# Kernel optimization log

Measured on AMD Instinct MI355X. Metric: run time of the kernel, lower is better.

The kernel has to match this reference:

```python
import jax, jax.numpy as jnp
import numpy as np

B, N, FN, FE, OUT = 64, 128, 64, 16, 128
S, VOCAB, EMB, LH = 1033, 1033, 50, 8
MOMO, SIDE, T = 200, 963, 3
LN_EPS, BN_EPS = 1e-12, 1e-5


def setup_inputs():
    key = jax.random.key(0)
    ks = iter(jax.random.split(key, 64))
    def nrm(shape, scale=0.05):
        return jax.random.normal(next(ks), shape, dtype=jnp.float32) * scale
    inp = {}
    inp['adjacency_1'] = (jax.random.uniform(next(ks), (B, N, N)) < 0.1).astype(jnp.float32)
    inp['nodes_1'] = nrm((B, N, FN), 1.0)
    inp['edges_1'] = nrm((B, N, N, FE), 1.0)
    inp['adjacency_2'] = (jax.random.uniform(next(ks), (B, N, N)) < 0.1).astype(jnp.float32)
    inp['nodes_2'] = nrm((B, N, FN), 1.0)
    inp['edges_2'] = nrm((B, N, N, FE), 1.0)
    inp['d1_momo_fts'] = nrm((B, MOMO), 1.0)
    inp['d2_momo_fts'] = nrm((B, MOMO), 1.0)
    inp['d1_protein_fts'] = jax.random.randint(next(ks), (B, S), 0, VOCAB)
    inp['d2_protein_fts'] = jax.random.randint(next(ks), (B, S), 0, VOCAB)
    inp['side_effect'] = nrm((B, SIDE), 1.0)
    inp['word_emb'] = nrm((VOCAB, EMB))
    inp['pos_emb'] = nrm((VOCAB, EMB))
    inp['ln_gamma'] = jnp.ones((EMB,), jnp.float32)
    inp['ln_beta'] = jnp.zeros((EMB,), jnp.float32)
    inp['W_ih'] = nrm((4 * LH, EMB))
    inp['W_hh'] = nrm((4 * LH, LH))
    inp['b_ih'] = jnp.zeros((4 * LH,), jnp.float32)
    inp['b_hh'] = jnp.zeros((4 * LH,), jnp.float32)
    inp['dec_W1'] = nrm((LH * S, 256))
    inp['dec_b1'] = jnp.zeros((256,), jnp.float32)
    inp['bn_gamma'] = jnp.ones((256,), jnp.float32)
    inp['bn_beta'] = jnp.zeros((256,), jnp.float32)
    inp['dec_W2'] = nrm((256, 45))
    inp['dec_b2'] = jnp.zeros((45,), jnp.float32)
    for g in ('1', '2'):
        inp['W_msg' + g] = nrm((FN, FN))
        inp['W_edge' + g] = nrm((FE, FN))
        inp['W_up' + g] = nrm((2 * FN, FN))
        inp['b_up' + g] = jnp.zeros((FN,), jnp.float32)
        inp['W_read' + g] = nrm((2 * FN, OUT))
        inp['b_read' + g] = jnp.zeros((OUT,), jnp.float32)
    inp['W_momo'] = nrm((MOMO, 45))
    inp['b_momo'] = jnp.zeros((45,), jnp.float32)
    inp['W_side'] = nrm((SIDE, 32))
    inp['b_side'] = jnp.zeros((32,), jnp.float32)
    inp['W_final'] = nrm((2 * (OUT + 45 + 45) + 32, 1))
    inp['b_final'] = jnp.zeros((1,), jnp.float32)
    return inp


def _mpnn(adj, nodes, edges, W_msg, W_edge, W_up, b_up, W_read, b_read):
    # Dense-masked equivalent of the padded neighbor/edge gather construction:
    # message[b,n] = sum_m adj[b,n,m] * (h[b,m] @ W_msg + e[b,n,m] @ W_edge)
    node_mask = adj.sum(-1) > 0  # [B,N] -- only connected nodes are updated
    edge_msg = jnp.einsum('bnm,bnmf,fk->bnk', adj, edges, W_edge)  # static over passes
    h = nodes
    for _ in range(T):
        msg = jnp.einsum('bnm,bmf,fk->bnk', adj, h, W_msg) + edge_msg
        upd = jax.nn.relu(jnp.concatenate([h, msg], -1) @ W_up + b_up)
        h = jnp.where(node_mask[..., None], upd, h)
    r = jax.nn.relu(jnp.concatenate([h, nodes], -1) @ W_read + b_read)  # [B,N,OUT]
    return jnp.einsum('bn,bnk->bk', node_mask.astype(h.dtype), r)


def _protein(ids, word_emb, pos_emb, ln_gamma, ln_beta, W_ih, W_hh, b_ih, b_hh,
             dec_W1, dec_b1, bn_gamma, bn_beta, dec_W2, dec_b2):
    x = word_emb[ids] + pos_emb[jnp.arange(S)][None]  # [B,S,EMB]
    u = x.mean(-1, keepdims=True)
    s = ((x - u) ** 2).mean(-1, keepdims=True)
    x = ln_gamma * (x - u) / jnp.sqrt(s + LN_EPS) + ln_beta
    def step(carry, xt):  # torch LSTM gate order: i, f, g, o
        h, c = carry
        gates = xt @ W_ih.T + b_ih + h @ W_hh.T + b_hh
        i, f, g, o = jnp.split(gates, 4, axis=-1)
        c = jax.nn.sigmoid(f) * c + jax.nn.sigmoid(i) * jnp.tanh(g)
        h = jax.nn.sigmoid(o) * jnp.tanh(c)
        return (h, c), h
    h0 = jnp.zeros((ids.shape[0], LH), jnp.float32)
    _, hs = jax.lax.scan(step, (h0, h0), jnp.swapaxes(x, 0, 1))  # [S,B,LH]
    p = jnp.swapaxes(hs, 0, 1).reshape(ids.shape[0], -1)  # [B, S*LH]
    p = jax.nn.relu(p @ dec_W1 + dec_b1)
    m, v = p.mean(0), p.var(0)  # BatchNorm1d in training mode (batch stats)
    p = bn_gamma * (p - m) / jnp.sqrt(v + BN_EPS) + bn_beta
    return p @ dec_W2 + dec_b2  # [B,45]


def reference(adjacency_1, nodes_1, edges_1, adjacency_2, nodes_2, edges_2,
              d1_momo_fts, d1_protein_fts, d2_momo_fts, d2_protein_fts, side_effect,
              word_emb, pos_emb, ln_gamma, ln_beta, W_ih, W_hh, b_ih, b_hh,
              dec_W1, dec_b1, bn_gamma, bn_beta, dec_W2, dec_b2,
              W_msg1, W_edge1, W_up1, b_up1, W_read1, b_read1,
              W_msg2, W_edge2, W_up2, b_up2, W_read2, b_read2,
              W_momo, b_momo, W_side, b_side, W_final, b_final):
    out1 = _mpnn(adjacency_1, nodes_1, edges_1, W_msg1, W_edge1, W_up1, b_up1, W_read1, b_read1)
    out2 = _mpnn(adjacency_2, nodes_2, edges_2, W_msg2, W_edge2, W_up2, b_up2, W_read2, b_read2)
    p1 = _protein(d1_protein_fts, word_emb, pos_emb, ln_gamma, ln_beta, W_ih, W_hh, b_ih, b_hh,
                  dec_W1, dec_b1, bn_gamma, bn_beta, dec_W2, dec_b2)
    p2 = _protein(d2_protein_fts, word_emb, pos_emb, ln_gamma, ln_beta, W_ih, W_hh, b_ih, b_hh,
                  dec_W1, dec_b1, bn_gamma, bn_beta, dec_W2, dec_b2)
    momo1 = d1_momo_fts @ W_momo + b_momo
    momo2 = d2_momo_fts @ W_momo + b_momo
    drug1 = jnp.concatenate([out1, p1, momo1], axis=1)
    drug2 = jnp.concatenate([out2, p2, momo2], axis=1)
    side = side_effect @ W_side + b_side
    feats = jnp.concatenate([drug1, drug2, side], axis=1)
    return feats @ W_final + b_final  # [B,1]
```

## Files before the change

kernel.cpp:

```cpp
#include <hip/hip_runtime.h>
#include <hip/hip_bf16.h>
#include <math.h>

#define Bb 64
#define Nn 128
#define FNf 64
#define Ss 1033
#define EMBe 50

typedef float f4 __attribute__((ext_vector_type(4)));
typedef float f2 __attribute__((ext_vector_type(2)));
typedef int   i4 __attribute__((ext_vector_type(4)));

#define HS_KSTRIDE 1036
#define HS_BSTRIDE 8288
#define HS_PSIZE   530432

constexpr size_t OFF_EMSG  = 2*524288 + 2*524288;
constexpr size_t OFF_MASK  = OFF_EMSG  + 2*524288;
constexpr size_t OFF_OUT12 = OFF_MASK  + 2*8192;
constexpr size_t OFF_PPRE  = OFF_OUT12 + 2*8192;
constexpr size_t OFF_PBN   = OFF_PPRE  + 2*16384;
constexpr size_t OFF_XW    = OFF_PBN   + 2*16384;
constexpr size_t OFF_HS    = OFF_XW    + 2*2115584;
constexpr size_t OFF_W2F   = OFF_HS    + 2*HS_PSIZE;
constexpr size_t OFF_WMF   = OFF_W2F   + 2*256;
constexpr size_t OFF_WSF   = OFF_WMF   + 2*200;
constexpr size_t OFF_CONST = OFF_WSF   + 964;
constexpr size_t OFF_COUNT = OFF_CONST + 4;
constexpr size_t OFF_NZ    = OFF_COUNT + 2*8192;
constexpr size_t OFF_AVAL  = OFF_NZ    + 2*524288;

__device__ inline f4 relu4(f4 v) {
  v[0] = fmaxf(v[0], 0.f); v[1] = fmaxf(v[1], 0.f);
  v[2] = fmaxf(v[2], 0.f); v[3] = fmaxf(v[3], 0.f);
  return v;
}

#define ROR16(x, n) __int_as_float(__builtin_amdgcn_update_dpp(0, __float_as_int(x), 0x120 + (n), 0xF, 0xF, true))

__global__ __launch_bounds__(256) void kA(
    const float* __restrict__ adj1, const float* __restrict__ adj2,
    const float* __restrict__ edges1, const float* __restrict__ edges2,
    const float* __restrict__ We1, const float* __restrict__ We2,
    const int* __restrict__ ids1, const int* __restrict__ ids2,
    const float* __restrict__ we, const float* __restrict__ pe,
    const float* __restrict__ lng, const float* __restrict__ lnb,
    const float* __restrict__ Wih, const float* __restrict__ bih,
    const float* __restrict__ bhh, float* __restrict__ ws) {
  int bid = blockIdx.x;
  int t = threadIdx.x;
  if (bid < 4096) {
    int g = bid >> 11;
    int w = t >> 6, lane = t & 63;
    int row = (bid & 2047) * 4 + w;
    const float* adj   = g ? adj2 : adj1;
    const float* edges = g ? edges2 : edges1;
    const float* We    = g ? We2 : We1;
    float* emsg  = ws + OFF_EMSG + (size_t)g * 524288;
    int*   cntg  = (int*)(ws + OFF_COUNT) + (size_t)g * 8192;
    int*   nz    = (int*)(ws + OFF_NZ)    + (size_t)g * 524288;
    float* aval  = ws + OFF_AVAL + (size_t)g * 524288;

    __shared__ int   lidx[4][64];
    __shared__ float lav[4][64];
    __shared__ float les[4][16];

    const float* arow = adj + (size_t)row * 128;
    float a0 = arow[lane], a1 = arow[64 + lane];
    unsigned long long m0 = __ballot(a0 != 0.f);
    unsigned long long m1 = __ballot(a1 != 0.f);
    int c0 = __popcll(m0);
    int cnt = c0 + __popcll(m1);
    unsigned long long below = ((unsigned long long)1 << lane) - 1ull;
    if (a0 != 0.f) { int pos = __popcll(m0 & below); if (pos < 64) { lidx[w][pos] = lane; lav[w][pos] = a0; } }
    if (a1 != 0.f) { int pos = c0 + __popcll(m1 & below); if (pos < 64) { lidx[w][pos] = lane + 64; lav[w][pos] = a1; } }
    int cc = cnt > 64 ? 64 : cnt;
    __syncthreads();

    nz[(size_t)row * 64 + lane]   = (lane < cc) ? lidx[w][lane] : 0;
    aval[(size_t)row * 64 + lane] = (lane < cc) ? lav[w][lane] : 0.f;

    int f = lane & 15, js = lane >> 4;
    float es = 0.f;
    const float* erow = edges + (size_t)row * 128 * 16;
    for (int j = js; j < cc; j += 4) es += lav[w][j] * erow[lidx[w][j] * 16 + f];
    es += __shfl_xor(es, 16);
    es += __shfl_xor(es, 32);
    if (lane < 16) les[w][lane] = es;
    __syncthreads();

    float acc = 0.f;
    #pragma unroll
    for (int ff = 0; ff < 16; ++ff) acc += les[w][ff] * We[ff * 64 + lane];
    emsg[(size_t)row * 64 + lane] = acc;
    if (lane == 0) cntg[row] = cc;
    return;
  }
  int bid6 = bid - 4096;
  int p = bid6 / 2066;
  int xb = bid6 % 2066;
  const int* ids = p ? ids2 : ids1;
  float* xw = ws + OFF_XW + (size_t)p * 2115584;
  __shared__ float wlds[1600];
  __shared__ float glds[50], blds[50], bs[32];
  __shared__ float xl6[8][52];
  for (int i = t; i < 1600; i += 256) wlds[i] = Wih[i];
  if (t < 50) { glds[t] = lng[t]; blds[t] = lnb[t]; }
  if (t < 32) bs[t] = bih[t] + bhh[t];
  __syncthreads();
  int grp = t >> 5, tl = t & 31;
  int newpos = (tl < 16) ? 2 * tl : 2 * tl - 31;
  const float L = 1.44269504088896f;
  float scale = (tl >= 16 && tl < 24) ? -2.f * L : -L;
  int q0 = xb * 32 + grp * 4;
  for (int qq = 0; qq < 4; ++qq) {
    int q = q0 + qq;
    int s = q % Ss;
    int id = ids[q];
    const float* wr = we + (size_t)id * 50;
    const float* pr = pe + (size_t)s * 50;
    float x1 = wr[tl] + pr[tl];
    bool has2 = (tl + 32) < 50;
    float x2 = has2 ? (wr[tl + 32] + pr[tl + 32]) : 0.f;
    float sm = x1 + x2, sq = x1 * x1 + x2 * x2;
    #pragma unroll
    for (int off = 16; off; off >>= 1) {
      sm += __shfl_xor(sm, off, 32);
      sq += __shfl_xor(sq, off, 32);
    }
    float u = sm * (1.f / 50.f);
    float var = fmaxf(sq * (1.f / 50.f) - u * u, 0.f);
    float rstd = rsqrtf(var + 1e-12f);
    xl6[grp][tl] = glds[tl] * (x1 - u) * rstd + blds[tl];
    if (has2) xl6[grp][tl + 32] = glds[tl + 32] * (x2 - u) * rstd + blds[tl + 32];
    __builtin_amdgcn_wave_barrier();
    float acc = bs[tl];
    #pragma unroll 10
    for (int k = 0; k < 50; ++k) acc += xl6[grp][k] * wlds[tl * 50 + k];
    xw[(size_t)q * 32 + newpos] = acc * scale;
    __builtin_amdgcn_wave_barrier();
  }
}

__global__ __launch_bounds__(256) void kB(
    const float* __restrict__ nodes1, const float* __restrict__ nodes2,
    const float* __restrict__ Wm1, const float* __restrict__ Wm2,
    const float* __restrict__ Wup1, const float* __restrict__ Wup2,
    const float* __restrict__ bup1, const float* __restrict__ bup2,
    const float* __restrict__ Wr1, const float* __restrict__ Wr2,
    const float* __restrict__ br1, const float* __restrict__ br2,
    const float* __restrict__ Whh, float* __restrict__ ws) {
  __shared__ __attribute__((aligned(16))) float hl[8192];
  __shared__ __attribute__((aligned(16))) float xl[8192];
  __shared__ __attribute__((aligned(16))) float wml[4096];
  __shared__ __attribute__((aligned(16))) float wbl[8192];
  int bid = blockIdx.x;
  int t = threadIdx.x;
  if (bid >= 128) {
    if (t >= 64) return;
    int idx = bid - 128;
    int p = idx >> 4, xb = idx & 15;
    const float* xw = ws + OFF_XW + (size_t)p * 2115584;
    float* hs = ws + OFF_HS + (size_t)p * HS_PSIZE;
    int lane16 = t & 15;
    int k = lane16 & 7;
    int half = lane16 >> 3;
    int b = xb * 4 + (t >> 4);
    const float* xwp = xw + (size_t)b * (Ss * 32) + lane16 * 2;
    float* hq = hs + (size_t)b * HS_BSTRIDE + (size_t)k * HS_KSTRIDE;
    const float L = 1.44269504088896f;
    int ga = half ? 8 + k : k;
    int gb = half ? 24 + k : 16 + k;
    float sb_scale = half ? -L : -2.f * L;
    float wa[8], wb[8];
    #pragma unroll
    for (int r = 0; r < 8; ++r) {
      int j = (k - r) & 7;
      wa[r] = -L * Whh[ga * 8 + j];
      wb[r] = sb_scale * Whh[gb * 8 + j];
    }
    float A = half ? 0.f : -4.f * L;
    float B = half ? 1.f : 2.f * L;
    float ho = 0.f, cs = 0.f;
    float q0v = 0.f, q1v = 0.f, q2v = 0.f, q3v = 0.f;

    f2 x[8];
    #pragma unroll
    for (int j = 0; j < 8; ++j) x[j] = *(const f2*)(xwp + (size_t)j * 32);
    const float* pf = xwp + 8 * 32;

    auto step = [&](f2 xc) {
      float h1 = ROR16(ho, 1);
      float h2 = ROR16(ho, 2);
      float h3 = ROR16(ho, 3);
      float h4 = ROR16(ho, 4);
      float h5 = ROR16(ho, 5);
      float h6 = ROR16(ho, 6);
      float h7 = ROR16(ho, 7);
      float a0 = fmaf(ho, wa[0], xc.x);
      float b0 = fmaf(ho, wb[0], xc.y);
      a0 = fmaf(h1, wa[1], a0);  b0 = fmaf(h1, wb[1], b0);
      a0 = fmaf(h2, wa[2], a0);  b0 = fmaf(h2, wb[2], b0);
      a0 = fmaf(h3, wa[3], a0);  b0 = fmaf(h3, wb[3], b0);
      float a1 = h4 * wa[4];     float b1 = h4 * wb[4];
      a1 = fmaf(h5, wa[5], a1);  b1 = fmaf(h5, wb[5], b1);
      a1 = fmaf(h6, wa[6], a1);  b1 = fmaf(h6, wb[6], b1);
      a1 = fmaf(h7, wa[7], a1);  b1 = fmaf(h7, wb[7], b1);
      float acc_a = a0 + a1;
      float acc_b = b0 + b1;
      float ea = __builtin_amdgcn_exp2f(acc_a);
      float sa = __builtin_amdgcn_rcpf(1.f + ea);
      float eb = __builtin_amdgcn_exp2f(acc_b);
      float tb = __builtin_amdgcn_rcpf(1.f + eb);
      float x_own = fmaf(sa * A, tb, sa * B);
      float x_oth = ROR16(x_own, 8);
      float t_oth = ROR16(tb, 8);
      float F  = half ? x_own : x_oth;
      float P2 = half ? x_oth : x_own;
      cs = fmaf(F, cs, P2);
      float e2 = __builtin_amdgcn_exp2f(cs);
      float tc = __builtin_amdgcn_rcpf(1.f + e2);
      float so = half ? tb : t_oth;
      ho = fmaf(so + so, tc, -so);
    };

    for (int g = 0; g < 129; ++g) {
      #pragma unroll
      for (int j = 0; j < 8; ++j) {
        f2 xc = x[j];
        x[j] = *(const f2*)(pf + j * 32);
        step(xc);
        if (j == 0 || j == 4) q0v = ho;
        else if (j == 1 || j == 5) q1v = ho;
        else if (j == 2 || j == 6) q2v = ho;
        else if (j == 3) { q3v = ho; if (!half) *(f4*)(hq + 0) = (f4){q0v, q1v, q2v, q3v}; }
        else { q3v = ho; if (!half) *(f4*)(hq + 4) = (f4){q0v, q1v, q2v, q3v}; }
      }
      pf += 256;
      hq += 8;
    }
    step(x[0]);
    if (!half) hq[0] = ho;
    return;
  }
  int g = bid >> 6, b = bid & 63;
  const float* nodes = g ? nodes2 : nodes1;
  const float* Wm  = g ? Wm2 : Wm1;
  const float* Wup = g ? Wup2 : Wup1;
  const float* bup = g ? bup2 : bup1;
  const float* Wr  = g ? Wr2 : Wr1;
  const float* br  = g ? br2 : br1;
  const float* emsg = ws + OFF_EMSG + (size_t)g * 524288;
  const int*   cntg = (const int*)(ws + OFF_COUNT) + (size_t)g * 8192;
  const int*   nz   = (const int*)(ws + OFF_NZ) + (size_t)g * 524288;
  const float* aval = ws + OFF_AVAL + (size_t)g * 524288;
  float* out12 = ws + OFF_OUT12 + (size_t)g * 8192;

  int col4 = (t & 15) * 4, rg = t >> 4;
  int r0 = rg * 8;
  for (int i = t; i < 4096; i += 256) wml[i] = Wm[i];
  for (int i = t; i < 8192; i += 256) wbl[i] = Wup[i];
  for (int i = t; i < 8192; i += 256) hl[i] = nodes[(size_t)b * 8192 + i];
  __syncthreads();

  for (int it = 0; it < 3; ++it) {
    {
      f4 acc[8];
      #pragma unroll
      for (int rr = 0; rr < 8; ++rr) acc[rr] = (f4){0.f, 0.f, 0.f, 0.f};
      for (int f0 = 0; f0 < 64; f0 += 4) {
        f4 h4[8];
        #pragma unroll
        for (int rr = 0; rr < 8; ++rr) h4[rr] = *(const f4*)&hl[(r0 + rr) * 64 + f0];
        #pragma unroll
        for (int ff = 0; ff < 4; ++ff) {
          f4 w4 = *(const f4*)&wml[(f0 + ff) * 64 + col4];
          #pragma unroll
          for (int rr = 0; rr < 8; ++rr) acc[rr] += h4[rr][ff] * w4;
        }
      }
      #pragma unroll
      for (int rr = 0; rr < 8; ++rr) *(f4*)&xl[(r0 + rr) * 64 + col4] = acc[rr];
    }
    __syncthreads();
    f4 msgv[8];
    #pragma unroll
    for (int rr = 0; rr < 8; ++rr) {
      int row = b * 128 + r0 + rr;
      f4 m = *(const f4*)&emsg[(size_t)row * 64 + col4];
      int cnt4 = (cntg[row] + 3) >> 2;
      const i4* nzr = (const i4*)(nz + (size_t)row * 64);
      const f4* avr = (const f4*)(aval + (size_t)row * 64);
      for (int j4 = 0; j4 < cnt4; ++j4) {
        i4 nq = nzr[j4];
        f4 aq = avr[j4];
        m += aq[0] * *(const f4*)&xl[nq[0] * 64 + col4];
        m += aq[1] * *(const f4*)&xl[nq[1] * 64 + col4];
        m += aq[2] * *(const f4*)&xl[nq[2] * 64 + col4];
        m += aq[3] * *(const f4*)&xl[nq[3] * 64 + col4];
      }
      msgv[rr] = m;
    }
    __syncthreads();
    #pragma unroll
    for (int rr = 0; rr < 8; ++rr) *(f4*)&xl[(r0 + rr) * 64 + col4] = msgv[rr];
    __syncthreads();
    {
      f4 u[8];
      #pragma unroll
      for (int rr = 0; rr < 8; ++rr) u[rr] = *(const f4*)&bup[col4];
      for (int f0 = 0; f0 < 64; f0 += 4) {
        f4 h4[8];
        #pragma unroll
        for (int rr = 0; rr < 8; ++rr) h4[rr] = *(const f4*)&hl[(r0 + rr) * 64 + f0];
        #pragma unroll
        for (int ff = 0; ff < 4; ++ff) {
          f4 w4 = *(const f4*)&wbl[(f0 + ff) * 64 + col4];
          #pragma unroll
          for (int rr = 0; rr < 8; ++rr) u[rr] += h4[rr][ff] * w4;
        }
      }
      for (int f0 = 0; f0 < 64; f0 += 4) {
        f4 m4[8];
        #pragma unroll
        for (int rr = 0; rr < 8; ++rr) m4[rr] = *(const f4*)&xl[(r0 + rr) * 64 + f0];
        #pragma unroll
        for (int ff = 0; ff < 4; ++ff) {
          f4 w4 = *(const f4*)&wbl[(64 + f0 + ff) * 64 + col4];
          #pragma unroll
          for (int rr = 0; rr < 8; ++rr) u[rr] += m4[rr][ff] * w4;
        }
      }
      __syncthreads();
      #pragma unroll
      for (int rr = 0; rr < 8; ++rr) {
        int row = b * 128 + r0 + rr;
        if (cntg[row] > 0) *(f4*)&hl[(r0 + rr) * 64 + col4] = relu4(u[rr]);
      }
    }
    __syncthreads();
  }

  for (int i = t; i < 8192; i += 256) xl[i] = nodes[(size_t)b * 8192 + i];
  __syncthreads();
  for (int kt = 0; kt < 2; ++kt) {
    for (int i = t; i < 8192; i += 256) {
      int f = i >> 6, c = i & 63;
      wbl[i] = Wr[f * 128 + kt * 64 + c];
    }
    __syncthreads();
    f4 part = {0.f, 0.f, 0.f, 0.f};
    {
      f4 u[8];
      #pragma unroll
      for (int rr = 0; rr < 8; ++rr) u[rr] = *(const f4*)&br[kt * 64 + col4];
      for (int f0 = 0; f0 < 64; f0 += 4) {
        f4 h4[8];
        #pragma unroll
        for (int rr = 0; rr < 8; ++rr) h4[rr] = *(const f4*)&hl[(r0 + rr) * 64 + f0];
        #pragma unroll
        for (int ff = 0; ff < 4; ++ff) {
          f4 w4 = *(const f4*)&wbl[(f0 + ff) * 64 + col4];
          #pragma unroll
          for (int rr = 0; rr < 8; ++rr) u[rr] += h4[rr][ff] * w4;
        }
      }
      for (int f0 = 0; f0 < 64; f0 += 4) {
        f4 n4[8];
        #pragma unroll
        for (int rr = 0; rr < 8; ++rr) n4[rr] = *(const f4*)&xl[(r0 + rr) * 64 + f0];
        #pragma unroll
        for (int ff = 0; ff < 4; ++ff) {
          f4 w4 = *(const f4*)&wbl[(64 + f0 + ff) * 64 + col4];
          #pragma unroll
          for (int rr = 0; rr < 8; ++rr) u[rr] += n4[rr][ff] * w4;
        }
      }
      #pragma unroll
      for (int rr = 0; rr < 8; ++rr) {
        int row = b * 128 + r0 + rr;
        if (cntg[row] > 0) part += relu4(u[rr]);
      }
    }
    *(f4*)&wml[rg * 64 + col4] = part;
    __syncthreads();
    for (int off = 8; off; off >>= 1) {
      if (rg < off) {
        f4 v = *(f4*)&wml[rg * 64 + col4] + *(f4*)&wml[(rg + off) * 64 + col4];
        *(f4*)&wml[rg * 64 + col4] = v;
      }
      __syncthreads();
    }
    if (rg == 0) *(f4*)&out12[(size_t)b * 128 + kt * 64 + col4] = *(f4*)&wml[col4];
    __syncthreads();
  }
}

__global__ __launch_bounds__(256) void kC(
    const float* __restrict__ W1,
    const float* __restrict__ W2, const float* __restrict__ b2,
    const float* __restrict__ Wm, const float* __restrict__ bm,
    const float* __restrict__ Wsd, const float* __restrict__ bsd,
    const float* __restrict__ Wf, const float* __restrict__ bf,
    float* __restrict__ ws) {
  int bid = blockIdx.x;
  int t = threadIdx.x;
  if (bid < 256) {
    int ks = bid & 31, jt = (bid >> 5) & 3, p = bid >> 7;
    const float* hs = ws + OFF_HS + (size_t)p * HS_PSIZE;
    float* pp = ws + OFF_PPRE + (size_t)p * 16384;
    int s0 = ks * 32;
    int s1 = (ks == 31) ? Ss : s0 + 32;
    int j0 = jt * 64;
    __shared__ __attribute__((aligned(16))) float hsl[4][768];
    __shared__ __attribute__((aligned(16))) float w1l[4][512];
    int jl = (t & 15) * 4, bb = t >> 4;
    f4 acc[4] = {};
    for (int sb = s0; sb < s1; sb += 4) {
      #pragma unroll
      for (int u = 0; u < 2; ++u) {
        int bk = t + 256 * u;
        int b = bk >> 3, k = bk & 7;
        f4 v = *(const f4*)&hs[(size_t)b * HS_BSTRIDE + (size_t)k * HS_KSTRIDE + sb];
        int c = b * 12 + k;
        hsl[0][c] = v[0]; hsl[1][c] = v[1]; hsl[2][c] = v[2]; hsl[3][c] = v[3];
      }
      #pragma unroll
      for (int u = 0; u < 2; ++u) {
        int idx = t + 256 * u;
        int ss = idx >> 7, l = (idx >> 4) & 7, jj = (idx & 15) * 4;
        int s = sb + ss;
        f4 wv = (s < Ss) ? *(const f4*)&W1[(size_t)(s * 8 + l) * 256 + j0 + jj]
                         : (f4){0.f, 0.f, 0.f, 0.f};
        *(f4*)&w1l[ss][l * 64 + jj] = wv;
      }
      __syncthreads();
      #pragma unroll
      for (int ss = 0; ss < 4; ++ss) {
        f4 r[4][2];
        #pragma unroll
        for (int i = 0; i < 4; ++i) {
          int b = bb + 16 * i;
          r[i][0] = *(const f4*)&hsl[ss][b * 12];
          r[i][1] = *(const f4*)&hsl[ss][b * 12 + 4];
        }
        #pragma unroll
        for (int l = 0; l < 8; ++l) {
          f4 wv = *(const f4*)&w1l[ss][l * 64 + jl];
          #pragma unroll
          for (int i = 0; i < 4; ++i) {
            float hv = (l < 4) ? r[i][0][l] : r[i][1][l - 4];
            acc[i] += hv * wv;
          }
        }
      }
      __syncthreads();
    }
    #pragma unroll
    for (int i = 0; i < 4; ++i) {
      int b = bb + 16 * i;
      float* dst = pp + (size_t)b * 256 + j0 + jl;
      atomicAdd(dst + 0, acc[i][0]); atomicAdd(dst + 1, acc[i][1]);
      atomicAdd(dst + 2, acc[i][2]); atomicAdd(dst + 3, acc[i][3]);
    }
    return;
  }
  __shared__ float wf[468];
  for (int i = t; i < 468; i += 256) wf[i] = Wf[i];
  __syncthreads();
  float* w2f = ws + OFF_W2F;
  float* wmf = ws + OFF_WMF;
  float* wsf = ws + OFF_WSF;
  float* cst = ws + OFF_CONST;
  {
    float a1 = 0.f, a2 = 0.f;
    for (int k = 0; k < 45; ++k) {
      float v = W2[t * 45 + k];
      a1 += v * wf[128 + k];
      a2 += v * wf[346 + k];
    }
    w2f[t] = a1; w2f[256 + t] = a2;
  }
  if (t < 200) {
    float a1 = 0.f, a2 = 0.f;
    for (int k = 0; k < 45; ++k) {
      float v = Wm[t * 45 + k];
      a1 += v * wf[173 + k];
      a2 += v * wf[391 + k];
    }
    wmf[t] = a1; wmf[200 + t] = a2;
  }
  for (int i = t; i < 963; i += 256) {
    float a = 0.f;
    for (int k = 0; k < 32; ++k) a += Wsd[i * 32 + k] * wf[436 + k];
    wsf[i] = a;
  }
  if (t == 0) {
    float cc = bf[0];
    for (int k = 0; k < 45; ++k)
      cc += b2[k] * (wf[128 + k] + wf[346 + k]) + bm[k] * (wf[173 + k] + wf[391 + k]);
    for (int k = 0; k < 32; ++k) cc += bsd[k] * wf[436 + k];
    cst[0] = cc;
  }
}

__global__ __launch_bounds__(256) void kD(
    const float* __restrict__ b1, const float* __restrict__ bng,
    const float* __restrict__ bnb,
    const float* __restrict__ d1m, const float* __restrict__ d2m,
    const float* __restrict__ se, const float* __restrict__ Wf,
    float* __restrict__ ws, float* __restrict__ out) {
  int b = blockIdx.x, t = threadIdx.x;
  const float* out12 = ws + OFF_OUT12;
  const float* pp0 = ws + OFF_PPRE;
  const float* pp1 = ws + OFF_PPRE + 16384;
  const float* w2f = ws + OFF_W2F;
  const float* wmf = ws + OFF_WMF;
  const float* wsf = ws + OFF_WSF;
  float bj = b1[t];
  float sm0 = 0.f, sq0 = 0.f, sm1 = 0.f, sq1 = 0.f;
  for (int bb = 0; bb < 64; ++bb) {
    float v0 = fmaxf(pp0[bb * 256 + t] + bj, 0.f);
    float v1 = fmaxf(pp1[bb * 256 + t] + bj, 0.f);
    sm0 += v0; sq0 += v0 * v0;
    sm1 += v1; sq1 += v1 * v1;
  }
  float m0 = sm0 * (1.f / 64.f);
  float var0 = fmaxf(sq0 * (1.f / 64.f) - m0 * m0, 0.f);
  float rstd0 = rsqrtf(var0 + 1e-5f);
  float sc0 = bng[t] * rstd0, sh0 = bnb[t] - m0 * sc0;
  float m1 = sm1 * (1.f / 64.f);
  float var1 = fmaxf(sq1 * (1.f / 64.f) - m1 * m1, 0.f);
  float rstd1 = rsqrtf(var1 + 1e-5f);
  float sc1 = bng[t] * rstd1, sh1 = bnb[t] - m1 * sc1;
  float val0 = sc0 * fmaxf(pp0[b * 256 + t] + bj, 0.f) + sh0;
  float val1 = sc1 * fmaxf(pp1[b * 256 + t] + bj, 0.f) + sh1;
  float acc = val0 * w2f[t] + val1 * w2f[256 + t];
  if (t < 128) {
    acc += out12[b * 128 + t] * Wf[t];
    acc += out12[8192 + b * 128 + t] * Wf[218 + t];
  }
  if (t < 200) {
    acc += d1m[b * 200 + t] * wmf[t];
    acc += d2m[b * 200 + t] * wmf[200 + t];
  }
  for (int i = t; i < 963; i += 256) acc += se[b * 963 + i] * wsf[i];
  __shared__ float red[256];
  red[t] = acc;
  __syncthreads();
  for (int off = 128; off; off >>= 1) {
    if (t < off) red[t] += red[t + off];
    __syncthreads();
  }
  if (t == 0) out[b] = red[0] + (ws + OFF_CONST)[0];
}

extern "C" void kernel_launch(void* const* d_in, const int* in_sizes, int n_in,
                              void* d_out, int out_size, void* d_ws, size_t ws_size,
                              hipStream_t stream) {
  const float* adj1  = (const float*)d_in[0];
  const float* nodes1= (const float*)d_in[1];
  const float* edges1= (const float*)d_in[2];
  const float* adj2  = (const float*)d_in[3];
  const float* nodes2= (const float*)d_in[4];
  const float* edges2= (const float*)d_in[5];
  const float* d1m   = (const float*)d_in[6];
  const float* d2m   = (const float*)d_in[7];
  const int*   ids1  = (const int*)d_in[8];
  const int*   ids2  = (const int*)d_in[9];
  const float* se    = (const float*)d_in[10];
  const float* we    = (const float*)d_in[11];
  const float* pe    = (const float*)d_in[12];
  const float* lng   = (const float*)d_in[13];
  const float* lnb   = (const float*)d_in[14];
  const float* Wih   = (const float*)d_in[15];
  const float* Whh   = (const float*)d_in[16];
  const float* bih   = (const float*)d_in[17];
  const float* bhh   = (const float*)d_in[18];
  const float* W1    = (const float*)d_in[19];
  const float* b1    = (const float*)d_in[20];
  const float* bng   = (const float*)d_in[21];
  const float* bnb   = (const float*)d_in[22];
  const float* W2    = (const float*)d_in[23];
  const float* b2    = (const float*)d_in[24];
  const float* Wm1   = (const float*)d_in[25];
  const float* We1   = (const float*)d_in[26];
  const float* Wup1  = (const float*)d_in[27];
  const float* bup1  = (const float*)d_in[28];
  const float* Wr1   = (const float*)d_in[29];
  const float* br1   = (const float*)d_in[30];
  const float* Wm2   = (const float*)d_in[31];
  const float* We2   = (const float*)d_in[32];
  const float* Wup2  = (const float*)d_in[33];
  const float* bup2  = (const float*)d_in[34];
  const float* Wr2   = (const float*)d_in[35];
  const float* br2   = (const float*)d_in[36];
  const float* Wmo   = (const float*)d_in[37];
  const float* bmo   = (const float*)d_in[38];
  const float* Wsd   = (const float*)d_in[39];
  const float* bsd   = (const float*)d_in[40];
  const float* Wf    = (const float*)d_in[41];
  const float* bf    = (const float*)d_in[42];
  float* ws = (float*)d_ws;
  float* out = (float*)d_out;

  hipMemsetAsync(ws + OFF_PPRE, 0, 2 * 16384 * sizeof(float), stream);

  kA<<<8228, 256, 0, stream>>>(adj1, adj2, edges1, edges2, We1, We2,
                               ids1, ids2, we, pe, lng, lnb, Wih, bih, bhh, ws);
  kB<<<160, 256, 0, stream>>>(nodes1, nodes2, Wm1, Wm2, Wup1, Wup2, bup1, bup2,
                              Wr1, Wr2, br1, br2, Whh, ws);
  kC<<<257, 256, 0, stream>>>(W1, W2, b2, Wmo, bmo, Wsd, bsd, Wf, bf, ws);
  kD<<<64, 256, 0, stream>>>(b1, bng, bnb, d1m, d2m, se, Wf, ws, out);
}
```

Before: 226.8 us.

## Overlap LSTM recurrence with decoder GEMM via progress flags; fold memset and fusion prep

The decoder W1 GEMM moves from a separate kernel into extra blocks of kB. These blocks spin on per-chunk progress counters that the LSTM recurrence blocks publish with release stores, so the GEMM can consume hidden states while the recurrence is still running. The small final-weight fusion precompute and the zeroing of the accumulation buffer move into extra kA blocks, which removes the memset and the kC launch. The price is spin-wait polling and a reliance on all 256 kB blocks being resident at once; without that the producer/consumer scheme could deadlock. The split-K tiling also goes from 32 to 12 chunks per slice, each covering more timesteps.

```diff
diff --git a/kernel.cpp b/kernel.cpp
--- a/kernel.cpp
+++ b/kernel.cpp
@@ -47,7 +47,12 @@
     const float* __restrict__ we, const float* __restrict__ pe,
     const float* __restrict__ lng, const float* __restrict__ lnb,
     const float* __restrict__ Wih, const float* __restrict__ bih,
-    const float* __restrict__ bhh, float* __restrict__ ws) {
+    const float* __restrict__ bhh,
+    const float* __restrict__ W2, const float* __restrict__ b2,
+    const float* __restrict__ Wm, const float* __restrict__ bm,
+    const float* __restrict__ Wsd, const float* __restrict__ bsd,
+    const float* __restrict__ Wf, const float* __restrict__ bf,
+    float* __restrict__ ws) {
   int bid = blockIdx.x;
   int t = threadIdx.x;
   if (bid < 4096) {
@@ -97,50 +102,100 @@
     if (lane == 0) cntg[row] = cc;
     return;
   }
-  int bid6 = bid - 4096;
-  int p = bid6 / 2066;
-  int xb = bid6 % 2066;
-  const int* ids = p ? ids2 : ids1;
-  float* xw = ws + OFF_XW + (size_t)p * 2115584;
-  __shared__ float wlds[1600];
-  __shared__ float glds[50], blds[50], bs[32];
-  __shared__ float xl6[8][52];
-  for (int i = t; i < 1600; i += 256) wlds[i] = Wih[i];
-  if (t < 50) { glds[t] = lng[t]; blds[t] = lnb[t]; }
-  if (t < 32) bs[t] = bih[t] + bhh[t];
-  __syncthreads();
-  int grp = t >> 5, tl = t & 31;
-  int newpos = (tl < 16) ? 2 * tl : 2 * tl - 31;
-  const float L = 1.44269504088896f;
-  float scale = (tl >= 16 && tl < 24) ? -2.f * L : -L;
-  int q0 = xb * 32 + grp * 4;
-  for (int qq = 0; qq < 4; ++qq) {
-    int q = q0 + qq;
-    int s = q % Ss;
-    int id = ids[q];
-    const float* wr = we + (size_t)id * 50;
-    const float* pr = pe + (size_t)s * 50;
-    float x1 = wr[tl] + pr[tl];
-    bool has2 = (tl + 32) < 50;
-    float x2 = has2 ? (wr[tl + 32] + pr[tl + 32]) : 0.f;
-    float sm = x1 + x2, sq = x1 * x1 + x2 * x2;
-    #pragma unroll
-    for (int off = 16; off; off >>= 1) {
-      sm += __shfl_xor(sm, off, 32);
-      sq += __shfl_xor(sq, off, 32);
-    }
-    float u = sm * (1.f / 50.f);
-    float var = fmaxf(sq * (1.f / 50.f) - u * u, 0.f);
-    float rstd = rsqrtf(var + 1e-12f);
-    xl6[grp][tl] = glds[tl] * (x1 - u) * rstd + blds[tl];
-    if (has2) xl6[grp][tl + 32] = glds[tl + 32] * (x2 - u) * rstd + blds[tl + 32];
-    __builtin_amdgcn_wave_barrier();
-    float acc = bs[tl];
-    #pragma unroll 10
-    for (int k = 0; k < 50; ++k) acc += xl6[grp][k] * wlds[tl * 50 + k];
-    xw[(size_t)q * 32 + newpos] = acc * scale;
-    __builtin_amdgcn_wave_barrier();
-  }
+  if (bid < 8228) {
+    int bid6 = bid - 4096;
+    int p = bid6 / 2066;
+    int xb = bid6 % 2066;
+    const int* ids = p ? ids2 : ids1;
+    float* xw = ws + OFF_XW + (size_t)p * 2115584;
+    __shared__ float wlds[1600];
+    __shared__ float glds[50], blds[50], bs[32];
+    __shared__ float xl6[8][52];
+    for (int i = t; i < 1600; i += 256) wlds[i] = Wih[i];
+    if (t < 50) { glds[t] = lng[t]; blds[t] = lnb[t]; }
+    if (t < 32) bs[t] = bih[t] + bhh[t];
+    __syncthreads();
+    int grp = t >> 5, tl = t & 31;
+    int newpos = (tl < 16) ? 2 * tl : 2 * tl - 31;
+    const float L = 1.44269504088896f;
+    float scale = (tl >= 16 && tl < 24) ? -2.f * L : -L;
+    int q0 = xb * 32 + grp * 4;
+    for (int qq = 0; qq < 4; ++qq) {
+      int q = q0 + qq;
+      int s = q % Ss;
+      int id = ids[q];
+      const float* wr = we + (size_t)id * 50;
+      const float* pr = pe + (size_t)s * 50;
+      float x1 = wr[tl] + pr[tl];
+      bool has2 = (tl + 32) < 50;
+      float x2 = has2 ? (wr[tl + 32] + pr[tl + 32]) : 0.f;
+      float sm = x1 + x2, sq = x1 * x1 + x2 * x2;
+      #pragma unroll
+      for (int off = 16; off; off >>= 1) {
+        sm += __shfl_xor(sm, off, 32);
+        sq += __shfl_xor(sq, off, 32);
+      }
+      float u = sm * (1.f / 50.f);
+      float var = fmaxf(sq * (1.f / 50.f) - u * u, 0.f);
+      float rstd = rsqrtf(var + 1e-12f);
+      xl6[grp][tl] = glds[tl] * (x1 - u) * rstd + blds[tl];
+      if (has2) xl6[grp][tl + 32] = glds[tl + 32] * (x2 - u) * rstd + blds[tl + 32];
+      __builtin_amdgcn_wave_barrier();
+      float acc = bs[tl];
+      #pragma unroll 10
+      for (int k = 0; k < 50; ++k) acc += xl6[grp][k] * wlds[tl * 50 + k];
+      xw[(size_t)q * 32 + newpos] = acc * scale;
+      __builtin_amdgcn_wave_barrier();
+    }
+    return;
+  }
+  if (bid == 8228) {
+    __shared__ float wf[468];
+    for (int i = t; i < 468; i += 256) wf[i] = Wf[i];
+    __syncthreads();
+    float* w2f = ws + OFF_W2F;
+    float* wmf = ws + OFF_WMF;
+    float* wsf = ws + OFF_WSF;
+    float* cst = ws + OFF_CONST;
+    {
+      float a1 = 0.f, a2 = 0.f;
+      for (int k = 0; k < 45; ++k) {
+        float v = W2[t * 45 + k];
+        a1 += v * wf[128 + k];
+        a2 += v * wf[346 + k];
+      }
+      w2f[t] = a1; w2f[256 + t] = a2;
+    }
+    if (t < 200) {
+      float a1 = 0.f, a2 = 0.f;
+      for (int k = 0; k < 45; ++k) {
+        float v = Wm[t * 45 + k];
+        a1 += v * wf[173 + k];
+        a2 += v * wf[391 + k];
+      }
+      wmf[t] = a1; wmf[200 + t] = a2;
+    }
+    for (int i = t; i < 963; i += 256) {
+      float a = 0.f;
+      for (int k = 0; k < 32; ++k) a += Wsd[i * 32 + k] * wf[436 + k];
+      wsf[i] = a;
+    }
+    if (t == 0) {
+      float cc = bf[0];
+      for (int k = 0; k < 45; ++k)
+        cc += b2[k] * (wf[128 + k] + wf[346 + k]) + bm[k] * (wf[173 + k] + wf[391 + k]);
+      for (int k = 0; k < 32; ++k) cc += bsd[k] * wf[436 + k];
+      cst[0] = cc;
+    }
+    return;
+  }
+  int z = bid - 8229;
+  float* pp = ws + OFF_PPRE;
+  f4 zz = {0.f, 0.f, 0.f, 0.f};
+  size_t basei = (size_t)z * 2048 + (size_t)t * 8;
+  *(f4*)&pp[basei] = zz;
+  *(f4*)&pp[basei + 4] = zz;
+  if (z == 0 && t < 64) ((int*)(ws + OFF_PBN))[t] = 0;
 }
 
 __global__ __launch_bounds__(256) void kB(
@@ -150,13 +205,87 @@
     const float* __restrict__ bup1, const float* __restrict__ bup2,
     const float* __restrict__ Wr1, const float* __restrict__ Wr2,
     const float* __restrict__ br1, const float* __restrict__ br2,
-    const float* __restrict__ Whh, float* __restrict__ ws) {
+    const float* __restrict__ Whh, const float* __restrict__ W1,
+    float* __restrict__ ws) {
   __shared__ __attribute__((aligned(16))) float hl[8192];
   __shared__ __attribute__((aligned(16))) float xl[8192];
   __shared__ __attribute__((aligned(16))) float wml[4096];
   __shared__ __attribute__((aligned(16))) float wbl[8192];
   int bid = blockIdx.x;
   int t = threadIdx.x;
+  int* prog = (int*)(ws + OFF_PBN);
+
+  if (bid >= 160) {
+    int cid = bid - 160;
+    int ks = cid % 12, jt = (cid / 12) % 4, p = cid / 48;
+    const float* hs = ws + OFF_HS + (size_t)p * HS_PSIZE;
+    float* pp = ws + OFF_PPRE + (size_t)p * 16384;
+    int s0 = ks * 92;
+    int s1 = (ks == 11) ? Ss : s0 + 92;
+    int j0 = jt * 64;
+    float* hsl = hl;
+    float* w1l = hl + 3072;
+    int jl = (t & 15) * 4, bb = t >> 4;
+    f4 acc[4] = {};
+    for (int sb = s0; sb < s1; sb += 4) {
+      if (((sb - s0) & 15) == 0) {
+        int need = sb + 16; if (need > Ss) need = Ss;
+        if (t < 16) {
+          while (__hip_atomic_load(&prog[p * 16 + t], __ATOMIC_ACQUIRE,
+                                   __HIP_MEMORY_SCOPE_AGENT) < need)
+            __builtin_amdgcn_s_sleep(8);
+        }
+        __syncthreads();
+      }
+      #pragma unroll
+      for (int u = 0; u < 2; ++u) {
+        int bk = t + 256 * u;
+        int b = bk >> 3, k = bk & 7;
+        f4 v = *(const f4*)&hs[(size_t)b * HS_BSTRIDE + (size_t)k * HS_KSTRIDE + sb];
+        int c = b * 12 + k;
+        hsl[0 * 768 + c] = v[0]; hsl[1 * 768 + c] = v[1];
+        hsl[2 * 768 + c] = v[2]; hsl[3 * 768 + c] = v[3];
+      }
+      #pragma unroll
+      for (int u = 0; u < 2; ++u) {
+        int idx = t + 256 * u;
+        int ss = idx >> 7, l = (idx >> 4) & 7, jj = (idx & 15) * 4;
+        int s = sb + ss;
+        f4 wv = (s < Ss) ? *(const f4*)&W1[(size_t)(s * 8 + l) * 256 + j0 + jj]
+                         : (f4){0.f, 0.f, 0.f, 0.f};
+        *(f4*)&w1l[ss * 512 + l * 64 + jj] = wv;
+      }
+      __syncthreads();
+      #pragma unroll
+      for (int ss = 0; ss < 4; ++ss) {
+        f4 r[4][2];
+        #pragma unroll
+        for (int i = 0; i < 4; ++i) {
+          int b = bb + 16 * i;
+          r[i][0] = *(const f4*)&hsl[ss * 768 + b * 12];
+          r[i][1] = *(const f4*)&hsl[ss * 768 + b * 12 + 4];
+        }
+        #pragma unroll
+        for (int l = 0; l < 8; ++l) {
+          f4 wv = *(const f4*)&w1l[ss * 512 + l * 64 + jl];
+          #pragma unroll
+          for (int i = 0; i < 4; ++i) {
+            float hv = (l < 4) ? r[i][0][l] : r[i][1][l - 4];
+            acc[i] += hv * wv;
+          }
+        }
+      }
+      __syncthreads();
+    }
+    #pragma unroll
+    for (int i = 0; i < 4; ++i) {
+      int b = bb + 16 * i;
+      float* dst = pp + (size_t)b * 256 + j0 + jl;
+      atomicAdd(dst + 0, acc[i][0]); atomicAdd(dst + 1, acc[i][1]);
+      atomicAdd(dst + 2, acc[i][2]); atomicAdd(dst + 3, acc[i][3]);
+    }
+    return;
+  }
   if (bid >= 128) {
     if (t >= 64) return;
     int idx = bid - 128;
@@ -239,9 +368,19 @@
       }
       pf += 256;
       hq += 8;
+      if ((g & 15) == 15 && t == 0) {
+        __threadfence();
+        __hip_atomic_store(&prog[idx], (g + 1) * 8, __ATOMIC_RELEASE,
+                           __HIP_MEMORY_SCOPE_AGENT);
+      }
     }
     step(x[0]);
     if (!half) hq[0] = ho;
+    if (t == 0) {
+      __threadfence();
+      __hip_atomic_store(&prog[idx], 1033, __ATOMIC_RELEASE,
+                         __HIP_MEMORY_SCOPE_AGENT);
+    }
     return;
   }
   int g = bid >> 6, b = bid & 63;
@@ -394,114 +533,6 @@
     }
     if (rg == 0) *(f4*)&out12[(size_t)b * 128 + kt * 64 + col4] = *(f4*)&wml[col4];
     __syncthreads();
-  }
-}
-
-__global__ __launch_bounds__(256) void kC(
-    const float* __restrict__ W1,
-    const float* __restrict__ W2, const float* __restrict__ b2,
-    const float* __restrict__ Wm, const float* __restrict__ bm,
-    const float* __restrict__ Wsd, const float* __restrict__ bsd,
-    const float* __restrict__ Wf, const float* __restrict__ bf,
-    float* __restrict__ ws) {
-  int bid = blockIdx.x;
-  int t = threadIdx.x;
-  if (bid < 256) {
-    int ks = bid & 31, jt = (bid >> 5) & 3, p = bid >> 7;
-    const float* hs = ws + OFF_HS + (size_t)p * HS_PSIZE;
-    float* pp = ws + OFF_PPRE + (size_t)p * 16384;
-    int s0 = ks * 32;
-    int s1 = (ks == 31) ? Ss : s0 + 32;
-    int j0 = jt * 64;
-    __shared__ __attribute__((aligned(16))) float hsl[4][768];
-    __shared__ __attribute__((aligned(16))) float w1l[4][512];
-    int jl = (t & 15) * 4, bb = t >> 4;
-    f4 acc[4] = {};
-    for (int sb = s0; sb < s1; sb += 4) {
-      #pragma unroll
-      for (int u = 0; u < 2; ++u) {
-        int bk = t + 256 * u;
-        int b = bk >> 3, k = bk & 7;
-        f4 v = *(const f4*)&hs[(size_t)b * HS_BSTRIDE + (size_t)k * HS_KSTRIDE + sb];
-        int c = b * 12 + k;
-        hsl[0][c] = v[0]; hsl[1][c] = v[1]; hsl[2][c] = v[2]; hsl[3][c] = v[3];
-      }
-      #pragma unroll
-      for (int u = 0; u < 2; ++u) {
-        int idx = t + 256 * u;
-        int ss = idx >> 7, l = (idx >> 4) & 7, jj = (idx & 15) * 4;
-        int s = sb + ss;
-        f4 wv = (s < Ss) ? *(const f4*)&W1[(size_t)(s * 8 + l) * 256 + j0 + jj]
-                         : (f4){0.f, 0.f, 0.f, 0.f};
-        *(f4*)&w1l[ss][l * 64 + jj] = wv;
-      }
-      __syncthreads();
-      #pragma unroll
-      for (int ss = 0; ss < 4; ++ss) {
-        f4 r[4][2];
-        #pragma unroll
-        for (int i = 0; i < 4; ++i) {
-          int b = bb + 16 * i;
-          r[i][0] = *(const f4*)&hsl[ss][b * 12];
-          r[i][1] = *(const f4*)&hsl[ss][b * 12 + 4];
-        }
-        #pragma unroll
-        for (int l = 0; l < 8; ++l) {
-          f4 wv = *(const f4*)&w1l[ss][l * 64 + jl];
-          #pragma unroll
-          for (int i = 0; i < 4; ++i) {
-            float hv = (l < 4) ? r[i][0][l] : r[i][1][l - 4];
-            acc[i] += hv * wv;
-          }
-        }
-      }
-      __syncthreads();
-    }
-    #pragma unroll
-    for (int i = 0; i < 4; ++i) {
-      int b = bb + 16 * i;
-      float* dst = pp + (size_t)b * 256 + j0 + jl;
-      atomicAdd(dst + 0, acc[i][0]); atomicAdd(dst + 1, acc[i][1]);
-      atomicAdd(dst + 2, acc[i][2]); atomicAdd(dst + 3, acc[i][3]);
-    }
-    return;
-  }
-  __shared__ float wf[468];
-  for (int i = t; i < 468; i += 256) wf[i] = Wf[i];
-  __syncthreads();
-  float* w2f = ws + OFF_W2F;
-  float* wmf = ws + OFF_WMF;
-  float* wsf = ws + OFF_WSF;
-  float* cst = ws + OFF_CONST;
-  {
-    float a1 = 0.f, a2 = 0.f;
-    for (int k = 0; k < 45; ++k) {
-      float v = W2[t * 45 + k];
-      a1 += v * wf[128 + k];
-      a2 += v * wf[346 + k];
-    }
-    w2f[t] = a1; w2f[256 + t] = a2;
-  }
-  if (t < 200) {
-    float a1 = 0.f, a2 = 0.f;
-    for (int k = 0; k < 45; ++k) {
-      float v = Wm[t * 45 + k];
-      a1 += v * wf[173 + k];
-      a2 += v * wf[391 + k];
-    }
-    wmf[t] = a1; wmf[200 + t] = a2;
-  }
-  for (int i = t; i < 963; i += 256) {
-    float a = 0.f;
-    for (int k = 0; k < 32; ++k) a += Wsd[i * 32 + k] * wf[436 + k];
-    wsf[i] = a;
-  }
-  if (t == 0) {
-    float cc = bf[0];
-    for (int k = 0; k < 45; ++k)
-      cc += b2[k] * (wf[128 + k] + wf[346 + k]) + bm[k] * (wf[173 + k] + wf[391 + k]);
-    for (int k = 0; k < 32; ++k) cc += bsd[k] * wf[436 + k];
-    cst[0] = cc;
   }
 }
 
@@ -605,12 +636,10 @@
   float* ws = (float*)d_ws;
   float* out = (float*)d_out;
 
-  hipMemsetAsync(ws + OFF_PPRE, 0, 2 * 16384 * sizeof(float), stream);
-
-  kA<<<8228, 256, 0, stream>>>(adj1, adj2, edges1, edges2, We1, We2,
-                               ids1, ids2, we, pe, lng, lnb, Wih, bih, bhh, ws);
-  kB<<<160, 256, 0, stream>>>(nodes1, nodes2, Wm1, Wm2, Wup1, Wup2, bup1, bup2,
-                              Wr1, Wr2, br1, br2, Whh, ws);
-  kC<<<257, 256, 0, stream>>>(W1, W2, b2, Wmo, bmo, Wsd, bsd, Wf, bf, ws);
+  kA<<<8245, 256, 0, stream>>>(adj1, adj2, edges1, edges2, We1, We2,
+                               ids1, ids2, we, pe, lng, lnb, Wih, bih, bhh,
+                               W2, b2, Wmo, bmo, Wsd, bsd, Wf, bf, ws);
+  kB<<<256, 256, 0, stream>>>(nodes1, nodes2, Wm1, Wm2, Wup1, Wup2, bup1, bup2,
+                              Wr1, Wr2, br1, br2, Whh, W1, ws);
   kD<<<64, 256, 0, stream>>>(b1, bng, bnb, d1m, d2m, se, Wf, ws, out);
 }
```

Result: slower. 304.3 us (+34.1%).
